# Optimization experiments

Hardware: AMD Instinct MI355X
Metric: run time of the kernel (lower is better)

Reference implementation:

```python
import jax, jax.numpy as jnp
import numpy as np

INPUT_SIZE = 24
OUTPUT_SIZE = 24
HIDDEN = 40
BATCH = 4096
SEQ = 256


def setup_inputs() -> dict:
    key = jax.random.key(0)
    ks = jax.random.split(key, 7)
    s = 1.0 / np.sqrt(HIDDEN)  # torch RNN/Linear default uniform bound
    x = jax.random.normal(ks[0], (BATCH, SEQ, INPUT_SIZE), dtype=jnp.float32)
    W_ih = jax.random.uniform(ks[1], (3 * HIDDEN, INPUT_SIZE), jnp.float32, -s, s)
    W_hh = jax.random.uniform(ks[2], (3 * HIDDEN, HIDDEN), jnp.float32, -s, s)
    b_ih = jax.random.uniform(ks[3], (3 * HIDDEN,), jnp.float32, -s, s)
    b_hh = jax.random.uniform(ks[4], (3 * HIDDEN,), jnp.float32, -s, s)
    W_fc = jax.random.uniform(ks[5], (OUTPUT_SIZE, HIDDEN), jnp.float32, -s, s)
    b_fc = jax.random.uniform(ks[6], (OUTPUT_SIZE,), jnp.float32, -s, s)
    return {"x": x, "W_ih": W_ih, "W_hh": W_hh, "b_ih": b_ih,
            "b_hh": b_hh, "W_fc": W_fc, "b_fc": b_fc}


def _gru_forward(x, W_ih, W_hh, b_ih, b_hh):
    # PyTorch GRU gate order: reset, update, new. Precompute input projections.
    B, T, _ = x.shape
    H = W_hh.shape[1]
    xg = jnp.einsum('bti,gi->btg', x, W_ih) + b_ih  # [B, T, 3H]

    def step(h, xg_t):
        hg = h @ W_hh.T + b_hh                      # [B, 3H]
        xr, xz, xn = jnp.split(xg_t, 3, axis=-1)
        hr, hz, hn = jnp.split(hg, 3, axis=-1)
        r = jax.nn.sigmoid(xr + hr)
        z = jax.nn.sigmoid(xz + hz)
        n = jnp.tanh(xn + r * hn)
        h_new = (1.0 - z) * n + z * h
        return h_new, h_new

    h0 = jnp.zeros((B, H), dtype=x.dtype)
    hT, outs = jax.lax.scan(step, h0, jnp.swapaxes(xg, 0, 1))  # outs: [T, B, H]
    return jnp.swapaxes(outs, 0, 1), hT                        # [B, T, H], [B, H]


def reference(x, W_ih, W_hh, b_ih, b_hh, W_fc, b_fc):
    seq_out, hT = _gru_forward(x, W_ih, W_hh, b_ih, b_hh)
    H = W_hh.shape[1]
    out = seq_out.reshape(-1, H)                   # [B*T, H]
    out = jax.nn.sigmoid(out @ W_fc.T + b_fc)      # [B*T, output_size]
    hidden = hT[None]                              # [n_layers=1, B, H]
    return out, hidden
```

## Files before the change

### kernel.cpp

```cpp
#include <hip/hip_runtime.h>
#include <math.h>

typedef __attribute__((ext_vector_type(8))) short short8;
typedef __attribute__((ext_vector_type(4))) float f32x4;

namespace {
constexpr int BATCH = 4096;
constexpr int SEQT  = 256;
constexpr int INSZ  = 24;
constexpr int H     = 40;
constexpr int NOUT  = 24;
constexpr int R     = 8;
constexpr int NT    = 256;

__device__ __forceinline__ unsigned short f2bf(float f) {
  unsigned int u = __float_as_uint(f);
  return (unsigned short)((u + 0x7FFFu + ((u >> 16) & 1u)) >> 16);
}
__device__ __forceinline__ unsigned short cvt_bf16(float f) {
  float r;
  asm("v_cvt_pk_bf16_f32 %0, %1, %2" : "=v"(r) : "v"(f), "v"(f));
  return (unsigned short)__float_as_uint(r);
}
__device__ __forceinline__ unsigned int cvt_pk2(float lo, float hi) {
  float r;
  asm("v_cvt_pk_bf16_f32 %0, %1, %2" : "=v"(r) : "v"(lo), "v"(hi));
  return __float_as_uint(r);
}
__device__ __forceinline__ float4 ld4(const float* p) {
  return *reinterpret_cast<const float4*>(p);
}
__device__ __forceinline__ float sigm(float v) {
  return __builtin_amdgcn_rcpf(1.0f + __builtin_amdgcn_exp2f(v * -1.442695041f));
}
__device__ __forceinline__ float tanh_fast(float v) {
  return fmaf(2.0f,
              __builtin_amdgcn_rcpf(1.0f + __builtin_amdgcn_exp2f(v * -2.885390082f)),
              -1.0f);
}
}

#define BAR()                                              \
  asm volatile("s_waitcnt lgkmcnt(0)" ::: "memory");       \
  __builtin_amdgcn_s_barrier();                            \
  __builtin_amdgcn_sched_barrier(0);

__global__ __launch_bounds__(NT) void gru_mfma4(
    const float* __restrict__ x, const float* __restrict__ Wih,
    const float* __restrict__ Whh, const float* __restrict__ bih,
    const float* __restrict__ bhh, const float* __restrict__ Wfc,
    const float* __restrict__ bfc, float* __restrict__ out,
    float* __restrict__ hid) {
  __shared__ __align__(16) unsigned short Abuf[2 * 1024];

  const int tid = threadIdx.x;
  const int l   = tid & 63;
  const int w   = tid >> 6;
  const int lm  = l & 15;
  const int lq  = l >> 4;
  const int gb0 = blockIdx.x * R;

  reinterpret_cast<uint4*>(Abuf)[tid] = make_uint4(0, 0, 0, 0);

  const int aBase0 = ((lm * 64 + lq * 8)      ^ ((lm & 7) << 3));
  const int aBase1 = ((lm * 64 + lq * 8 + 32) ^ ((lm & 7) << 3));

  short8 B[4][2];
  float bias[4] = {0, 0, 0, 0};
  float hold[2] = {0, 0};
  int aw[2] = {0, 0};
  int u = 0;
  bool gvalid = false;
  if (w < 3) {
    u = w * 16 + lm;
    gvalid = (u < H);
#pragma unroll
    for (int z = 0; z < 4; ++z) {
#pragma unroll
      for (int kt = 0; kt < 2; ++kt) {
        short8 b;
#pragma unroll
        for (int j = 0; j < 8; ++j) {
          const int k = kt * 32 + lq * 8 + j;
          float v = 0.0f;
          if (gvalid) {
            if (z == 0)      v = (k < 24) ? Wih[u * 24 + k]          : Whh[u * 40 + (k - 24)];
            else if (z == 1) v = (k < 24) ? Wih[(40 + u) * 24 + k]   : Whh[(40 + u) * 40 + (k - 24)];
            else if (z == 2) v = (k < 24) ? Wih[(80 + u) * 24 + k]   : 0.0f;
            else             v = (k < 24) ? 0.0f                     : Whh[(80 + u) * 40 + (k - 24)];
          }
          b[j] = (short)f2bf(v);
        }
        B[z][kt] = b;
      }
    }
    if (gvalid) {
      bias[0] = bih[u] + bhh[u];
      bias[1] = bih[40 + u] + bhh[40 + u];
      bias[2] = bih[80 + u];
      bias[3] = bhh[80 + u];
    }
#pragma unroll
    for (int i = 0; i < 2; ++i) {
      const int arow = lq * 4 + i;
      aw[i] = ((arow * 64 + 24 + u) ^ ((arow & 7) << 3));
    }
  }

  short8 F[2][2];
  float biasF[2] = {0, 0};
  float* orow[2] = {nullptr, nullptr};
  const float* xp0 = nullptr;
  int xw0 = 0;
  bool xv = false;
  float4 xQ1 = make_float4(0,0,0,0), xQ2 = make_float4(0,0,0,0);
  float4 xQ3 = make_float4(0,0,0,0), xQ0 = make_float4(0,0,0,0);
  if (w == 3) {
#pragma unroll
    for (int f = 0; f < 2; ++f) {
      const int o = f * 16 + lm;
#pragma unroll
      for (int kt = 0; kt < 2; ++kt) {
        short8 b;
#pragma unroll
        for (int j = 0; j < 8; ++j) {
          const int k = kt * 32 + lq * 8 + j;
          const float v = (o < NOUT && k >= 24) ? Wfc[o * H + (k - 24)] : 0.0f;
          b[j] = (short)f2bf(v);
        }
        F[f][kt] = b;
      }
      biasF[f] = (o < NOUT) ? bfc[o] : 0.0f;
    }
#pragma unroll
    for (int i = 0; i < 2; ++i)
      orow[i] = out + ((size_t)(gb0 + lq * 2 + i) * SEQT) * NOUT;

    xv = (l < 48);
    const int xr = l / 6, xc = (l - xr * 6) * 4;
    const int ar_ = ((xr >> 1) << 2) + (xr & 1);
    if (xv) xp0 = x + ((size_t)(gb0 + xr) * SEQT) * INSZ + xc;
    xw0 = ((ar_ * 64 + xc) ^ ((ar_ & 7) << 3));
  }

  const f32x4 kZero = {0.0f, 0.0f, 0.0f, 0.0f};

  __syncthreads();

  if (w == 3 && xv) {
    const float4 v0 = ld4(xp0);
    *reinterpret_cast<uint2*>(&Abuf[xw0]) =
        make_uint2(cvt_pk2(v0.x, v0.y), cvt_pk2(v0.z, v0.w));
    xQ1 = ld4(xp0 + 1 * INSZ);
    xQ2 = ld4(xp0 + 2 * INSZ);
    xQ3 = ld4(xp0 + 3 * INSZ);
    xQ0 = ld4(xp0 + 4 * INSZ);
  }
  __syncthreads();

#define GATE_STEP(BO, NBO)                                                      \
  if (w < 3) {                                                                  \
    const short8 A0 = *reinterpret_cast<const short8*>(&Abuf[(BO) + aBase0]);   \
    const short8 A1 = *reinterpret_cast<const short8*>(&Abuf[(BO) + aBase1]);   \
    f32x4 ar = __builtin_amdgcn_mfma_f32_16x16x32_bf16(A0, B[0][0], kZero, 0, 0, 0); \
    f32x4 az = __builtin_amdgcn_mfma_f32_16x16x32_bf16(A0, B[1][0], kZero, 0, 0, 0); \
    f32x4 ax = __builtin_amdgcn_mfma_f32_16x16x32_bf16(A0, B[2][0], kZero, 0, 0, 0); \
    f32x4 ah = __builtin_amdgcn_mfma_f32_16x16x32_bf16(A0, B[3][0], kZero, 0, 0, 0); \
    ar = __builtin_amdgcn_mfma_f32_16x16x32_bf16(A1, B[0][1], ar, 0, 0, 0);     \
    az = __builtin_amdgcn_mfma_f32_16x16x32_bf16(A1, B[1][1], az, 0, 0, 0);     \
    ah = __builtin_amdgcn_mfma_f32_16x16x32_bf16(A1, B[3][1], ah, 0, 0, 0);     \
    _Pragma("unroll")                                                           \
    for (int i = 0; i < 2; ++i) {                                               \
      const float rr = sigm(ar[i] + bias[0]);                                   \
      const float zz = sigm(az[i] + bias[1]);                                   \
      const float nn = tanh_fast(fmaf(rr, ah[i] + bias[3], ax[i] + bias[2]));   \
      const float h  = fmaf(zz, hold[i] - nn, nn);                              \
      hold[i] = h;                                                              \
      if (gvalid) Abuf[(NBO) + aw[i]] = cvt_bf16(h);                            \
    }                                                                           \
  }

#define XSTAGE(T, TBO, XS)                                                      \
  if (xv) {                                                                     \
    if ((T) < SEQT) {                                                           \
      *reinterpret_cast<uint2*>(&Abuf[(TBO) + xw0]) =                           \
          make_uint2(cvt_pk2(XS.x, XS.y), cvt_pk2(XS.z, XS.w));                 \
    }                                                                           \
    if ((T) + 4 < SEQT) XS = ld4(xp0 + (size_t)((T) + 4) * INSZ);               \
  }

#define FC_STEP(T, BO)                                                          \
  {                                                                             \
    const short8 hA0 = *reinterpret_cast<const short8*>(&Abuf[(BO) + aBase0]);  \
    const short8 hA1 = *reinterpret_cast<const short8*>(&Abuf[(BO) + aBase1]);  \
    f32x4 f0 = __builtin_amdgcn_mfma_f32_16x16x32_bf16(hA0, F[0][0], kZero, 0, 0, 0); \
    f32x4 f1 = __builtin_amdgcn_mfma_f32_16x16x32_bf16(hA0, F[1][0], kZero, 0, 0, 0); \
    f0 = __builtin_amdgcn_mfma_f32_16x16x32_bf16(hA1, F[0][1], f0, 0, 0, 0);    \
    f1 = __builtin_amdgcn_mfma_f32_16x16x32_bf16(hA1, F[1][1], f1, 0, 0, 0);    \
    _Pragma("unroll")                                                           \
    for (int i = 0; i < 2; ++i) {                                               \
      orow[i][(size_t)(T) * NOUT + lm] = sigm(f0[i] + biasF[0]);                \
      if (lm < 8) orow[i][(size_t)(T) * NOUT + 16 + lm] = sigm(f1[i] + biasF[1]); \
    }                                                                           \
  }

  for (int tt = 0; tt < SEQT; tt += 4) {
    GATE_STEP(0, 1024)
    if (w == 3) {
      XSTAGE(tt + 1, 1024, xQ1)
      if (tt > 0) FC_STEP(tt - 1, 0)
    }
    BAR()
    GATE_STEP(1024, 0)
    if (w == 3) {
      XSTAGE(tt + 2, 0, xQ2)
      FC_STEP(tt, 1024)
    }
    BAR()
    GATE_STEP(0, 1024)
    if (w == 3) {
      XSTAGE(tt + 3, 1024, xQ3)
      FC_STEP(tt + 1, 0)
    }
    BAR()
    GATE_STEP(1024, 0)
    if (w == 3) {
      XSTAGE(tt + 4, 0, xQ0)
      FC_STEP(tt + 2, 1024)
    }
    BAR()
  }
  if (w == 3) FC_STEP(SEQT - 1, 0)

  if (w < 3 && gvalid) {
#pragma unroll
    for (int i = 0; i < 2; ++i)
      hid[(size_t)(gb0 + lq * 2 + i) * H + u] = hold[i];
  }
}

extern "C" void kernel_launch(void* const* d_in, const int* in_sizes, int n_in,
                              void* d_out, int out_size, void* d_ws, size_t ws_size,
                              hipStream_t stream) {
  const float* x   = (const float*)d_in[0];
  const float* Wih = (const float*)d_in[1];
  const float* Whh = (const float*)d_in[2];
  const float* bih = (const float*)d_in[3];
  const float* bhh = (const float*)d_in[4];
  const float* Wfc = (const float*)d_in[5];
  const float* bfc = (const float*)d_in[6];
  float* out = (float*)d_out;
  float* hid = out + (size_t)BATCH * SEQT * NOUT;

  dim3 grid(BATCH / R);
  dim3 block(NT);
  hipLaunchKernelGGL(gru_mfma4, grid, block, 0, stream,
                     x, Wih, Whh, bih, bhh, Wfc, bfc, out, hid);
}
```

Measured before the change: 112.6 us.

## Process two independent batch groups per block for ILP in GRU recurrence

Each block now handles 16 batch rows as two independent groups of 8, interleaving their MFMA chains, gate math, x staging and FC output within the same barrier-synchronised timestep loop. The aim is to hide MFMA and transcendental latency on the serial recurrence by giving each wave two independent dependency chains, and to halve the number of per-step barriers per batch row. In exchange the grid shrinks to 256 blocks, which lowers CU occupancy across the device, and LDS and register use double.

```diff
diff --git a/kernel.cpp b/kernel.cpp
--- a/kernel.cpp
+++ b/kernel.cpp
@@ -10,7 +10,7 @@
 constexpr int INSZ  = 24;
 constexpr int H     = 40;
 constexpr int NOUT  = 24;
-constexpr int R     = 8;
+constexpr int R     = 16;
 constexpr int NT    = 256;
 
 __device__ __forceinline__ unsigned short f2bf(float f) {
@@ -45,13 +45,15 @@
   __builtin_amdgcn_s_barrier();                            \
   __builtin_amdgcn_sched_barrier(0);
 
-__global__ __launch_bounds__(NT) void gru_mfma4(
+#define MFMA16(A, Bf, C) __builtin_amdgcn_mfma_f32_16x16x32_bf16((A), (Bf), (C), 0, 0, 0)
+
+__global__ __launch_bounds__(NT) void gru_ilp2(
     const float* __restrict__ x, const float* __restrict__ Wih,
     const float* __restrict__ Whh, const float* __restrict__ bih,
     const float* __restrict__ bhh, const float* __restrict__ Wfc,
     const float* __restrict__ bfc, float* __restrict__ out,
     float* __restrict__ hid) {
-  __shared__ __align__(16) unsigned short Abuf[2 * 1024];
+  __shared__ __align__(16) unsigned short Abuf[4 * 1024];
 
   const int tid = threadIdx.x;
   const int l   = tid & 63;
@@ -60,14 +62,15 @@
   const int lq  = l >> 4;
   const int gb0 = blockIdx.x * R;
 
-  reinterpret_cast<uint4*>(Abuf)[tid] = make_uint4(0, 0, 0, 0);
+  reinterpret_cast<uint4*>(Abuf)[tid]       = make_uint4(0, 0, 0, 0);
+  reinterpret_cast<uint4*>(Abuf)[tid + 256] = make_uint4(0, 0, 0, 0);
 
   const int aBase0 = ((lm * 64 + lq * 8)      ^ ((lm & 7) << 3));
   const int aBase1 = ((lm * 64 + lq * 8 + 32) ^ ((lm & 7) << 3));
 
   short8 B[4][2];
   float bias[4] = {0, 0, 0, 0};
-  float hold[2] = {0, 0};
+  float hold[2][2] = {{0, 0}, {0, 0}};
   int aw[2] = {0, 0};
   int u = 0;
   bool gvalid = false;
@@ -109,12 +112,14 @@
 
   short8 F[2][2];
   float biasF[2] = {0, 0};
-  float* orow[2] = {nullptr, nullptr};
-  const float* xp0 = nullptr;
+  float* orow[2][2] = {{nullptr, nullptr}, {nullptr, nullptr}};
+  const float* xpg[2] = {nullptr, nullptr};
   int xw0 = 0;
   bool xv = false;
-  float4 xQ1 = make_float4(0,0,0,0), xQ2 = make_float4(0,0,0,0);
-  float4 xQ3 = make_float4(0,0,0,0), xQ0 = make_float4(0,0,0,0);
+  float4 aQ1 = make_float4(0,0,0,0), aQ2 = make_float4(0,0,0,0);
+  float4 aQ3 = make_float4(0,0,0,0), aQ0 = make_float4(0,0,0,0);
+  float4 bQ1 = make_float4(0,0,0,0), bQ2 = make_float4(0,0,0,0);
+  float4 bQ3 = make_float4(0,0,0,0), bQ0 = make_float4(0,0,0,0);
   if (w == 3) {
 #pragma unroll
     for (int f = 0; f < 2; ++f) {
@@ -133,13 +138,18 @@
       biasF[f] = (o < NOUT) ? bfc[o] : 0.0f;
     }
 #pragma unroll
-    for (int i = 0; i < 2; ++i)
-      orow[i] = out + ((size_t)(gb0 + lq * 2 + i) * SEQT) * NOUT;
+    for (int g = 0; g < 2; ++g)
+#pragma unroll
+      for (int i = 0; i < 2; ++i)
+        orow[g][i] = out + ((size_t)(gb0 + g * 8 + lq * 2 + i) * SEQT) * NOUT;
 
     xv = (l < 48);
     const int xr = l / 6, xc = (l - xr * 6) * 4;
     const int ar_ = ((xr >> 1) << 2) + (xr & 1);
-    if (xv) xp0 = x + ((size_t)(gb0 + xr) * SEQT) * INSZ + xc;
+    if (xv) {
+      xpg[0] = x + ((size_t)(gb0 + xr) * SEQT) * INSZ + xc;
+      xpg[1] = x + ((size_t)(gb0 + 8 + xr) * SEQT) * INSZ + xc;
+    }
     xw0 = ((ar_ * 64 + xc) ^ ((ar_ & 7) << 3));
   }
 
@@ -148,94 +158,132 @@
   __syncthreads();
 
   if (w == 3 && xv) {
-    const float4 v0 = ld4(xp0);
+    const float4 v0 = ld4(xpg[0]);
     *reinterpret_cast<uint2*>(&Abuf[xw0]) =
         make_uint2(cvt_pk2(v0.x, v0.y), cvt_pk2(v0.z, v0.w));
-    xQ1 = ld4(xp0 + 1 * INSZ);
-    xQ2 = ld4(xp0 + 2 * INSZ);
-    xQ3 = ld4(xp0 + 3 * INSZ);
-    xQ0 = ld4(xp0 + 4 * INSZ);
+    const float4 v1 = ld4(xpg[1]);
+    *reinterpret_cast<uint2*>(&Abuf[2048 + xw0]) =
+        make_uint2(cvt_pk2(v1.x, v1.y), cvt_pk2(v1.z, v1.w));
+    aQ1 = ld4(xpg[0] + 1 * INSZ);  bQ1 = ld4(xpg[1] + 1 * INSZ);
+    aQ2 = ld4(xpg[0] + 2 * INSZ);  bQ2 = ld4(xpg[1] + 2 * INSZ);
+    aQ3 = ld4(xpg[0] + 3 * INSZ);  bQ3 = ld4(xpg[1] + 3 * INSZ);
+    aQ0 = ld4(xpg[0] + 4 * INSZ);  bQ0 = ld4(xpg[1] + 4 * INSZ);
   }
   __syncthreads();
 
-#define GATE_STEP(BO, NBO)                                                      \
+#define GATE2(BO, NBO)                                                          \
   if (w < 3) {                                                                  \
-    const short8 A0 = *reinterpret_cast<const short8*>(&Abuf[(BO) + aBase0]);   \
-    const short8 A1 = *reinterpret_cast<const short8*>(&Abuf[(BO) + aBase1]);   \
-    f32x4 ar = __builtin_amdgcn_mfma_f32_16x16x32_bf16(A0, B[0][0], kZero, 0, 0, 0); \
-    f32x4 az = __builtin_amdgcn_mfma_f32_16x16x32_bf16(A0, B[1][0], kZero, 0, 0, 0); \
-    f32x4 ax = __builtin_amdgcn_mfma_f32_16x16x32_bf16(A0, B[2][0], kZero, 0, 0, 0); \
-    f32x4 ah = __builtin_amdgcn_mfma_f32_16x16x32_bf16(A0, B[3][0], kZero, 0, 0, 0); \
-    ar = __builtin_amdgcn_mfma_f32_16x16x32_bf16(A1, B[0][1], ar, 0, 0, 0);     \
-    az = __builtin_amdgcn_mfma_f32_16x16x32_bf16(A1, B[1][1], az, 0, 0, 0);     \
-    ah = __builtin_amdgcn_mfma_f32_16x16x32_bf16(A1, B[3][1], ah, 0, 0, 0);     \
+    const short8 A00 = *reinterpret_cast<const short8*>(&Abuf[(BO) + aBase0]);  \
+    const short8 A01 = *reinterpret_cast<const short8*>(&Abuf[(BO) + aBase1]);  \
+    const short8 A10 = *reinterpret_cast<const short8*>(&Abuf[2048 + (BO) + aBase0]); \
+    const short8 A11 = *reinterpret_cast<const short8*>(&Abuf[2048 + (BO) + aBase1]); \
+    f32x4 ar0 = MFMA16(A00, B[0][0], kZero);                                    \
+    f32x4 az0 = MFMA16(A00, B[1][0], kZero);                                    \
+    f32x4 ax0 = MFMA16(A00, B[2][0], kZero);                                    \
+    f32x4 ah0 = MFMA16(A00, B[3][0], kZero);                                    \
+    f32x4 ar1 = MFMA16(A10, B[0][0], kZero);                                    \
+    f32x4 az1 = MFMA16(A10, B[1][0], kZero);                                    \
+    f32x4 ax1 = MFMA16(A10, B[2][0], kZero);                                    \
+    f32x4 ah1 = MFMA16(A10, B[3][0], kZero);                                    \
+    ar0 = MFMA16(A01, B[0][1], ar0);                                            \
+    az0 = MFMA16(A01, B[1][1], az0);                                            \
+    ah0 = MFMA16(A01, B[3][1], ah0);                                            \
+    ar1 = MFMA16(A11, B[0][1], ar1);                                            \
+    az1 = MFMA16(A11, B[1][1], az1);                                            \
+    ah1 = MFMA16(A11, B[3][1], ah1);                                            \
     _Pragma("unroll")                                                           \
     for (int i = 0; i < 2; ++i) {                                               \
-      const float rr = sigm(ar[i] + bias[0]);                                   \
-      const float zz = sigm(az[i] + bias[1]);                                   \
-      const float nn = tanh_fast(fmaf(rr, ah[i] + bias[3], ax[i] + bias[2]));   \
-      const float h  = fmaf(zz, hold[i] - nn, nn);                              \
-      hold[i] = h;                                                              \
+      const float rr = sigm(ar0[i] + bias[0]);                                  \
+      const float zz = sigm(az0[i] + bias[1]);                                  \
+      const float nn = tanh_fast(fmaf(rr, ah0[i] + bias[3], ax0[i] + bias[2])); \
+      const float h  = fmaf(zz, hold[0][i] - nn, nn);                           \
+      hold[0][i] = h;                                                           \
       if (gvalid) Abuf[(NBO) + aw[i]] = cvt_bf16(h);                            \
     }                                                                           \
-  }
-
-#define XSTAGE(T, TBO, XS)                                                      \
+    _Pragma("unroll")                                                           \
+    for (int i = 0; i < 2; ++i) {                                               \
+      const float rr = sigm(ar1[i] + bias[0]);                                  \
+      const float zz = sigm(az1[i] + bias[1]);                                  \
+      const float nn = tanh_fast(fmaf(rr, ah1[i] + bias[3], ax1[i] + bias[2])); \
+      const float h  = fmaf(zz, hold[1][i] - nn, nn);                           \
+      hold[1][i] = h;                                                           \
+      if (gvalid) Abuf[2048 + (NBO) + aw[i]] = cvt_bf16(h);                     \
+    }                                                                           \
+  }
+
+#define XSTAGE2(T, TBO, XSa, XSb)                                               \
   if (xv) {                                                                     \
     if ((T) < SEQT) {                                                           \
       *reinterpret_cast<uint2*>(&Abuf[(TBO) + xw0]) =                           \
-          make_uint2(cvt_pk2(XS.x, XS.y), cvt_pk2(XS.z, XS.w));                 \
-    }                                                                           \
-    if ((T) + 4 < SEQT) XS = ld4(xp0 + (size_t)((T) + 4) * INSZ);               \
-  }
-
-#define FC_STEP(T, BO)                                                          \
+          make_uint2(cvt_pk2(XSa.x, XSa.y), cvt_pk2(XSa.z, XSa.w));             \
+      *reinterpret_cast<uint2*>(&Abuf[2048 + (TBO) + xw0]) =                    \
+          make_uint2(cvt_pk2(XSb.x, XSb.y), cvt_pk2(XSb.z, XSb.w));             \
+    }                                                                           \
+    if ((T) + 4 < SEQT) {                                                       \
+      XSa = ld4(xpg[0] + (size_t)((T) + 4) * INSZ);                             \
+      XSb = ld4(xpg[1] + (size_t)((T) + 4) * INSZ);                             \
+    }                                                                           \
+  }
+
+#define FC2(T, BO)                                                              \
   {                                                                             \
-    const short8 hA0 = *reinterpret_cast<const short8*>(&Abuf[(BO) + aBase0]);  \
-    const short8 hA1 = *reinterpret_cast<const short8*>(&Abuf[(BO) + aBase1]);  \
-    f32x4 f0 = __builtin_amdgcn_mfma_f32_16x16x32_bf16(hA0, F[0][0], kZero, 0, 0, 0); \
-    f32x4 f1 = __builtin_amdgcn_mfma_f32_16x16x32_bf16(hA0, F[1][0], kZero, 0, 0, 0); \
-    f0 = __builtin_amdgcn_mfma_f32_16x16x32_bf16(hA1, F[0][1], f0, 0, 0, 0);    \
-    f1 = __builtin_amdgcn_mfma_f32_16x16x32_bf16(hA1, F[1][1], f1, 0, 0, 0);    \
+    const short8 hA00 = *reinterpret_cast<const short8*>(&Abuf[(BO) + aBase0]); \
+    const short8 hA01 = *reinterpret_cast<const short8*>(&Abuf[(BO) + aBase1]); \
+    const short8 hA10 = *reinterpret_cast<const short8*>(&Abuf[2048 + (BO) + aBase0]); \
+    const short8 hA11 = *reinterpret_cast<const short8*>(&Abuf[2048 + (BO) + aBase1]); \
+    f32x4 f00 = MFMA16(hA00, F[0][0], kZero);                                   \
+    f32x4 f01 = MFMA16(hA00, F[1][0], kZero);                                   \
+    f32x4 f10 = MFMA16(hA10, F[0][0], kZero);                                   \
+    f32x4 f11 = MFMA16(hA10, F[1][0], kZero);                                   \
+    f00 = MFMA16(hA01, F[0][1], f00);                                           \
+    f01 = MFMA16(hA01, F[1][1], f01);                                           \
+    f10 = MFMA16(hA11, F[0][1], f10);                                           \
+    f11 = MFMA16(hA11, F[1][1], f11);                                           \
     _Pragma("unroll")                                                           \
     for (int i = 0; i < 2; ++i) {                                               \
-      orow[i][(size_t)(T) * NOUT + lm] = sigm(f0[i] + biasF[0]);                \
-      if (lm < 8) orow[i][(size_t)(T) * NOUT + 16 + lm] = sigm(f1[i] + biasF[1]); \
+      orow[0][i][(size_t)(T) * NOUT + lm] = sigm(f00[i] + biasF[0]);            \
+      orow[1][i][(size_t)(T) * NOUT + lm] = sigm(f10[i] + biasF[0]);            \
+      if (lm < 8) {                                                             \
+        orow[0][i][(size_t)(T) * NOUT + 16 + lm] = sigm(f01[i] + biasF[1]);     \
+        orow[1][i][(size_t)(T) * NOUT + 16 + lm] = sigm(f11[i] + biasF[1]);     \
+      }                                                                         \
     }                                                                           \
   }
 
   for (int tt = 0; tt < SEQT; tt += 4) {
-    GATE_STEP(0, 1024)
+    GATE2(0, 1024)
     if (w == 3) {
-      XSTAGE(tt + 1, 1024, xQ1)
-      if (tt > 0) FC_STEP(tt - 1, 0)
+      XSTAGE2(tt + 1, 1024, aQ1, bQ1)
+      if (tt > 0) FC2(tt - 1, 0)
     }
     BAR()
-    GATE_STEP(1024, 0)
+    GATE2(1024, 0)
     if (w == 3) {
-      XSTAGE(tt + 2, 0, xQ2)
-      FC_STEP(tt, 1024)
+      XSTAGE2(tt + 2, 0, aQ2, bQ2)
+      FC2(tt, 1024)
     }
     BAR()
-    GATE_STEP(0, 1024)
+    GATE2(0, 1024)
     if (w == 3) {
-      XSTAGE(tt + 3, 1024, xQ3)
-      FC_STEP(tt + 1, 0)
+      XSTAGE2(tt + 3, 1024, aQ3, bQ3)
+      FC2(tt + 1, 0)
     }
     BAR()
-    GATE_STEP(1024, 0)
+    GATE2(1024, 0)
     if (w == 3) {
-      XSTAGE(tt + 4, 0, xQ0)
-      FC_STEP(tt + 2, 1024)
+      XSTAGE2(tt + 4, 0, aQ0, bQ0)
+      FC2(tt + 2, 1024)
     }
     BAR()
   }
-  if (w == 3) FC_STEP(SEQT - 1, 0)
+  if (w == 3) FC2(SEQT - 1, 0)
 
   if (w < 3 && gvalid) {
 #pragma unroll
-    for (int i = 0; i < 2; ++i)
-      hid[(size_t)(gb0 + lq * 2 + i) * H + u] = hold[i];
+    for (int g = 0; g < 2; ++g)
+#pragma unroll
+      for (int i = 0; i < 2; ++i)
+        hid[(size_t)(gb0 + g * 8 + lq * 2 + i) * H + u] = hold[g][i];
   }
 }
 
@@ -254,6 +302,6 @@
 
   dim3 grid(BATCH / R);
   dim3 block(NT);
-  hipLaunchKernelGGL(gru_mfma4, grid, block, 0, stream,
+  hipLaunchKernelGGL(gru_ilp2, grid, block, 0, stream,
                      x, Wih, Whh, bih, bhh, Wfc, bfc, out, hid);
 }
```

After: 138.0 us. 22.6% more time.
